# Performance work log

Hardware: AMD Instinct MI355X
Metric: run time of the kernel (lower is better)

Reference implementation:

```python
import jax, jax.numpy as jnp
import numpy as np

B, S, E, H = 1, 2048, 1024, 16
D = E // H          # head_dim = 64
SM_SCALE = 0.5      # module default, not 1/sqrt(D)


def setup_inputs() -> dict:
    key = jax.random.key(0)
    ks = jax.random.split(key, 9)
    std = 0.02
    return {
        "x":  jax.random.normal(ks[0], (B, S, E), dtype=jnp.float32),
        "Wq": jax.random.normal(ks[1], (E, E), dtype=jnp.float32) * std,
        "bq": jnp.zeros((E,), dtype=jnp.float32),
        "Wk": jax.random.normal(ks[2], (E, E), dtype=jnp.float32) * std,
        "bk": jnp.zeros((E,), dtype=jnp.float32),
        "Wv": jax.random.normal(ks[3], (E, E), dtype=jnp.float32) * std,
        "bv": jnp.zeros((E,), dtype=jnp.float32),
        "Wo": jax.random.normal(ks[4], (E, E), dtype=jnp.float32) * std,
        "bo": jnp.zeros((E,), dtype=jnp.float32),
    }


def _split_heads(t):
    # [B,S,E] -> [B,H,S,D]
    b, s, _ = t.shape
    return jnp.transpose(t.reshape(b, s, H, D), (0, 2, 1, 3))


def reference(x, Wq, bq, Wk, bk, Wv, bv, Wo, bo):
    # Projections in fp32, then cast to bf16 (matches module's .astype(bf16))
    q = _split_heads((x @ Wq + bq).astype(jnp.bfloat16))
    k = _split_heads((x @ Wk + bk).astype(jnp.bfloat16))
    v = _split_heads((x @ Wv + bv).astype(jnp.bfloat16))

    # Blockwise loop in the original is mathematically full causal attention
    scores = jnp.einsum("bhqd,bhkd->bhqk", q, k) * SM_SCALE  # [B,H,S,S] bf16
    causal = jnp.tril(jnp.ones((S, S), dtype=bool))
    scores = jnp.where(causal[None, None, :, :], scores, -jnp.inf)
    probs = jax.nn.softmax(scores, axis=-1)
    out = jnp.einsum("bhqk,bhkd->bhqd", probs, v)            # [B,H,S,D]

    out = jnp.transpose(out, (0, 2, 1, 3)).reshape(B, S, E)
    # dropout off (is_training=False / rate=0); final projection in fp32
    return out.astype(jnp.float32) @ Wo + bo
```

## Files before the change

### kernel.cpp

```cpp
#include <hip/hip_runtime.h>
#include <hip/hip_bf16.h>

#define S_LEN 2048
#define E_DIM 1024
#define NH    16
#define HD    64
#define SM_SCALE 0.5f

typedef short bf16x8_t __attribute__((ext_vector_type(8)));
typedef float f32x4_t  __attribute__((ext_vector_type(4)));
typedef __bf16 bf16x4_t __attribute__((ext_vector_type(4)));

static __device__ __forceinline__ unsigned short f2bf_bits(float f) {
    return __builtin_bit_cast(unsigned short, (__bf16)f);
}

#define GLD16(gp, lp) __builtin_amdgcn_global_load_lds(                       \
    (const __attribute__((address_space(1))) void*)(gp),                      \
    (__attribute__((address_space(3))) void*)(lp), 16, 0, 0)

__global__ void k_prep(const float* __restrict__ x,
                       const float* __restrict__ Wq, const float* __restrict__ Wk,
                       const float* __restrict__ Wv, const float* __restrict__ Wo,
                       __bf16* __restrict__ xb, __bf16* __restrict__ wt) {
    const int z = blockIdx.z;
    if (z < 4) {
        __shared__ float tile[32][33];
        const float* W = z == 0 ? Wq : z == 1 ? Wk : z == 2 ? Wv : Wo;
        __bf16* o = wt + (size_t)z * E_DIM * E_DIM;
        const int tx = threadIdx.x, ty = threadIdx.y;
        const int bx = blockIdx.x * 32, by = blockIdx.y * 32;
#pragma unroll
        for (int j = 0; j < 32; j += 8)
            tile[ty + j][tx] = W[(size_t)(by + ty + j) * E_DIM + bx + tx];
        __syncthreads();
#pragma unroll
        for (int j = 0; j < 32; j += 8)
            o[(size_t)(bx + ty + j) * E_DIM + by + tx] = (__bf16)tile[tx][ty + j];
    } else {
        const int bid = (z - 4) * 1024 + blockIdx.y * 32 + blockIdx.x;
        const int tid = threadIdx.y * 32 + threadIdx.x;
        const int i = bid * 256 + tid;
        const float4 v = ((const float4*)x)[i];
        bf16x4_t o4;
        o4.x = (__bf16)v.x; o4.y = (__bf16)v.y; o4.z = (__bf16)v.z; o4.w = (__bf16)v.w;
        ((bf16x4_t*)xb)[i] = o4;
    }
}

__global__ __launch_bounds__(256) void k_gemm_qkv(
    const __bf16* __restrict__ xb, const __bf16* __restrict__ wt,
    const float* __restrict__ bq, const float* __restrict__ bk, const float* __restrict__ bv,
    __bf16* __restrict__ qkv) {
    __shared__ __align__(16) unsigned short As[64 * 32];
    __shared__ __align__(16) unsigned short Bs[128 * 32];

    const int z = blockIdx.z;
    const __bf16* Bt = wt + (size_t)z * E_DIM * E_DIM;
    const float* bias = z == 0 ? bq : z == 1 ? bk : bv;
    __bf16* out = qkv + (size_t)z * NH * S_LEN * HD;

    const int tid = threadIdx.x, w = tid >> 6, l = tid & 63;
    const int lm = l & 15, q4 = l >> 4;
    const int bm = blockIdx.y, bn = blockIdx.x;
    const int wm = w >> 1, wn = w & 1;

    const int sm = (w << 4) + (l >> 2);
    const int skk = (l & 3) << 3;
    const __bf16* Ag = xb + (size_t)(bm * 64 + sm) * E_DIM + skk;
    const __bf16* Bg = Bt + (size_t)(bn * 128 + sm) * E_DIM + skk;
    unsigned short* AsW = As + (w << 9);
    unsigned short* BsW = Bs + (w << 9);

    f32x4_t acc[2][4];
#pragma unroll
    for (int i = 0; i < 2; i++)
#pragma unroll
        for (int j = 0; j < 4; j++) { acc[i][j].x = 0.f; acc[i][j].y = 0.f; acc[i][j].z = 0.f; acc[i][j].w = 0.f; }

    for (int k0 = 0; k0 < E_DIM; k0 += 32) {
        __syncthreads();
        GLD16(Ag + k0, AsW);
        GLD16(Bg + k0, BsW);
        GLD16(Bg + (size_t)64 * E_DIM + k0, BsW + 2048);
        __syncthreads();

        bf16x8_t af[2], bfr[4];
#pragma unroll
        for (int mt = 0; mt < 2; mt++)
            af[mt] = *(const bf16x8_t*)&As[(wm * 32 + mt * 16 + lm) * 32 + q4 * 8];
#pragma unroll
        for (int nt = 0; nt < 4; nt++)
            bfr[nt] = *(const bf16x8_t*)&Bs[(wn * 64 + nt * 16 + lm) * 32 + q4 * 8];
#pragma unroll
        for (int mt = 0; mt < 2; mt++)
#pragma unroll
            for (int nt = 0; nt < 4; nt++)
                acc[mt][nt] = __builtin_amdgcn_mfma_f32_16x16x32_bf16(af[mt], bfr[nt], acc[mt][nt], 0, 0, 0);
    }

#pragma unroll
    for (int nt = 0; nt < 4; nt++) {
        const int n = bn * 128 + wn * 64 + nt * 16 + lm;
        const float bval = bias[n];
        const int h = n >> 6, d = n & 63;
        if (z == 2) {
            __bf16* ob = out + (size_t)h * HD * S_LEN + (size_t)d * S_LEN;
#pragma unroll
            for (int mt = 0; mt < 2; mt++) {
                const int r0 = bm * 64 + wm * 32 + mt * 16 + q4 * 4;
                union { unsigned short s[4]; uint2 u; } pk;
#pragma unroll
                for (int i = 0; i < 4; i++) pk.s[i] = f2bf_bits(acc[mt][nt][i] + bval);
                *(uint2*)(ob + r0) = pk.u;
            }
        } else {
            const float scale = (z == 0) ? SM_SCALE : 1.0f;
            __bf16* ob = out + (size_t)h * S_LEN * HD + d;
#pragma unroll
            for (int mt = 0; mt < 2; mt++) {
                const int r0 = bm * 64 + wm * 32 + mt * 16 + q4 * 4;
#pragma unroll
                for (int i = 0; i < 4; i++)
                    ob[(size_t)(r0 + i) * HD] = (__bf16)((acc[mt][nt][i] + bval) * scale);
            }
        }
    }
}

__global__ __launch_bounds__(256, 2) void k_attn(
    const __bf16* __restrict__ Q, const __bf16* __restrict__ K, const __bf16* __restrict__ Vt,
    __bf16* __restrict__ attn) {
    __shared__ __align__(16) unsigned short KV[4 * 4096];
    __shared__ __align__(16) unsigned short Pl[4][32 * 72];

    const int b = blockIdx.x;
    int qt, h;
    if (b < 256) { qt = 16 + (b >> 4); h = b & 15; }
    else         { qt = 15 - ((b - 256) >> 4); h = (b - 256) & 15; }

    const int tid = threadIdx.x, w = tid >> 6, l = tid & 63;
    const int p = w & 1;
    const int rh = w >> 1;
    const int lm = l & 15, q4 = l >> 4;

    const __bf16* Qb = Q + (size_t)h * S_LEN * HD;
    const __bf16* Kb = K + (size_t)h * S_LEN * HD;
    const __bf16* Vb = Vt + (size_t)h * HD * S_LEN;

    const int qrow0 = qt * 64 + rh * 32;

    bf16x8_t qf[2][2];
#pragma unroll
    for (int rg = 0; rg < 2; rg++)
#pragma unroll
        for (int c = 0; c < 2; c++)
            qf[rg][c] = *(const bf16x8_t*)(Qb + (size_t)(qrow0 + rg * 16 + lm) * HD + c * 32 + q4 * 8);

    float lacc[2][4];
    f32x4_t oacc[2][4];
#pragma unroll
    for (int rg = 0; rg < 2; rg++)
#pragma unroll
        for (int i = 0; i < 4; i++) lacc[rg][i] = 0.f;
#pragma unroll
    for (int rg = 0; rg < 2; rg++)
#pragma unroll
        for (int t = 0; t < 4; t++) { oacc[rg][t].x = 0.f; oacc[rg][t].y = 0.f; oacc[rg][t].z = 0.f; oacc[rg][t].w = 0.f; }

    unsigned short* Pw = Pl[w];
    unsigned short* stg = KV + (w << 12);
    const int swz = (l & 7) ^ (l >> 3);

    const int nsteps = qt / 2 + 1;
    for (int s = 0; s < nsteps; s++) {
        __syncthreads();
        {
            const int tkt = 2 * s + (w & 1);
            if (w < 2) {
                const __bf16* gp = Kb + (size_t)tkt * 64 * HD;
#pragma unroll
                for (int i = 0; i < 8; i++)
                    GLD16(gp + (size_t)(i * 8 + (l >> 3)) * HD + swz * 8,
                          stg + i * 512 + l * 8);
            } else {
                const __bf16* gp = Vb + (size_t)tkt * 64;
#pragma unroll
                for (int i = 0; i < 8; i++)
                    GLD16(gp + (size_t)(i * 8 + (l >> 3)) * S_LEN + swz * 8,
                          stg + i * 512 + l * 8);
            }
        }
        __syncthreads();

        const int kt = 2 * s + p;
        if (kt > qt) continue;
        const unsigned short* Ksp = KV + p * 4096;
        const unsigned short* Vsp = KV + (2 + p) * 4096;

        f32x4_t sc[2][4];
#pragma unroll
        for (int rg = 0; rg < 2; rg++)
#pragma unroll
            for (int t = 0; t < 4; t++) { sc[rg][t].x = 0.f; sc[rg][t].y = 0.f; sc[rg][t].z = 0.f; sc[rg][t].w = 0.f; }
#pragma unroll
        for (int t = 0; t < 4; t++) {
            const int row = t * 16 + lm;
            bf16x8_t kf0 = *(const bf16x8_t*)&Ksp[row * 64 + ((q4 ^ (lm & 7)) << 3)];
            bf16x8_t kf1 = *(const bf16x8_t*)&Ksp[row * 64 + (((4 + q4) ^ (lm & 7)) << 3)];
            sc[0][t] = __builtin_amdgcn_mfma_f32_16x16x32_bf16(qf[0][0], kf0, sc[0][t], 0, 0, 0);
            sc[0][t] = __builtin_amdgcn_mfma_f32_16x16x32_bf16(qf[0][1], kf1, sc[0][t], 0, 0, 0);
            sc[1][t] = __builtin_amdgcn_mfma_f32_16x16x32_bf16(qf[1][0], kf0, sc[1][t], 0, 0, 0);
            sc[1][t] = __builtin_amdgcn_mfma_f32_16x16x32_bf16(qf[1][1], kf1, sc[1][t], 0, 0, 0);
        }
        if (kt == qt) {
#pragma unroll
            for (int rg = 0; rg < 2; rg++)
#pragma unroll
                for (int t = 0; t < 4; t++) {
                    const int kcol = kt * 64 + t * 16 + lm;
#pragma unroll
                    for (int i = 0; i < 4; i++) {
                        const int qrow = qrow0 + rg * 16 + q4 * 4 + i;
                        sc[rg][t][i] = (kcol > qrow) ? 0.f : __expf(sc[rg][t][i]);
                    }
                }
        } else {
#pragma unroll
            for (int rg = 0; rg < 2; rg++)
#pragma unroll
                for (int t = 0; t < 4; t++)
#pragma unroll
                    for (int i = 0; i < 4; i++) sc[rg][t][i] = __expf(sc[rg][t][i]);
        }
#pragma unroll
        for (int rg = 0; rg < 2; rg++)
#pragma unroll
            for (int i = 0; i < 4; i++)
                lacc[rg][i] += (sc[rg][0][i] + sc[rg][1][i]) + (sc[rg][2][i] + sc[rg][3][i]);
#pragma unroll
        for (int rg = 0; rg < 2; rg++)
#pragma unroll
            for (int t = 0; t < 4; t++)
#pragma unroll
                for (int i = 0; i < 4; i++)
                    Pw[(rg * 16 + q4 * 4 + i) * 72 + t * 16 + lm] = f2bf_bits(sc[rg][t][i]);
#pragma unroll
        for (int c = 0; c < 2; c++) {
            bf16x8_t pf0 = *(const bf16x8_t*)&Pw[lm * 72 + c * 32 + q4 * 8];
            bf16x8_t pf1 = *(const bf16x8_t*)&Pw[(16 + lm) * 72 + c * 32 + q4 * 8];
#pragma unroll
            for (int t = 0; t < 4; t++) {
                bf16x8_t vf = *(const bf16x8_t*)&Vsp[(t * 16 + lm) * 64 + ((((c << 2) + q4) ^ (lm & 7)) << 3)];
                oacc[0][t] = __builtin_amdgcn_mfma_f32_16x16x32_bf16(pf0, vf, oacc[0][t], 0, 0, 0);
                oacc[1][t] = __builtin_amdgcn_mfma_f32_16x16x32_bf16(pf1, vf, oacc[1][t], 0, 0, 0);
            }
        }
    }

    __syncthreads();
    float* Ex = (float*)KV;
    float* Ll = (float*)Pl;
    if (p == 1) {
#pragma unroll
        for (int rg = 0; rg < 2; rg++)
#pragma unroll
            for (int t = 0; t < 4; t++)
#pragma unroll
                for (int i = 0; i < 4; i++) {
                    const int idx = rg * 16 + t * 4 + i;
                    Ex[(rh * 64 + l) * 32 + ((idx + l) & 31)] = oacc[rg][t][i];
                }
#pragma unroll
        for (int rg = 0; rg < 2; rg++)
#pragma unroll
            for (int i = 0; i < 4; i++)
                Ll[(rh * 64 + l) * 8 + rg * 4 + i] = lacc[rg][i];
    }
    __syncthreads();
    if (p == 0) {
#pragma unroll
        for (int rg = 0; rg < 2; rg++)
#pragma unroll
            for (int t = 0; t < 4; t++)
#pragma unroll
                for (int i = 0; i < 4; i++) {
                    const int idx = rg * 16 + t * 4 + i;
                    oacc[rg][t][i] += Ex[(rh * 64 + l) * 32 + ((idx + l) & 31)];
                }
#pragma unroll
        for (int rg = 0; rg < 2; rg++)
#pragma unroll
            for (int i = 0; i < 4; i++)
                lacc[rg][i] += Ll[(rh * 64 + l) * 8 + rg * 4 + i];
#pragma unroll
        for (int off = 1; off <= 8; off <<= 1)
#pragma unroll
            for (int rg = 0; rg < 2; rg++)
#pragma unroll
                for (int i = 0; i < 4; i++)
                    lacc[rg][i] += __shfl_xor(lacc[rg][i], off, 64);
#pragma unroll
        for (int rg = 0; rg < 2; rg++)
#pragma unroll
            for (int i = 0; i < 4; i++) {
                const float rl = 1.f / lacc[rg][i];
                const int row = qrow0 + rg * 16 + q4 * 4 + i;
#pragma unroll
                for (int t = 0; t < 4; t++)
                    attn[(size_t)row * E_DIM + h * HD + t * 16 + lm] = (__bf16)(oacc[rg][t][i] * rl);
            }
    }
}

__global__ __launch_bounds__(256) void k_gemm_out(
    const __bf16* __restrict__ A, const __bf16* __restrict__ Bt,
    const float* __restrict__ bias, float* __restrict__ out) {
    __shared__ __align__(16) unsigned short As[64 * 32];
    __shared__ __align__(16) unsigned short Bs[128 * 32];

    const int tid = threadIdx.x, w = tid >> 6, l = tid & 63;
    const int lm = l & 15, q4 = l >> 4;
    const int bm = blockIdx.y, bn = blockIdx.x;
    const int wm = w >> 1, wn = w & 1;

    const int sm = (w << 4) + (l >> 2);
    const int skk = (l & 3) << 3;
    const __bf16* Ag = A + (size_t)(bm * 64 + sm) * E_DIM + skk;
    const __bf16* Bg = Bt + (size_t)(bn * 128 + sm) * E_DIM + skk;
    unsigned short* AsW = As + (w << 9);
    unsigned short* BsW = Bs + (w << 9);

    f32x4_t acc[2][4];
#pragma unroll
    for (int i = 0; i < 2; i++)
#pragma unroll
        for (int j = 0; j < 4; j++) { acc[i][j].x = 0.f; acc[i][j].y = 0.f; acc[i][j].z = 0.f; acc[i][j].w = 0.f; }

    for (int k0 = 0; k0 < E_DIM; k0 += 32) {
        __syncthreads();
        GLD16(Ag + k0, AsW);
        GLD16(Bg + k0, BsW);
        GLD16(Bg + (size_t)64 * E_DIM + k0, BsW + 2048);
        __syncthreads();

        bf16x8_t af[2], bfr[4];
#pragma unroll
        for (int mt = 0; mt < 2; mt++)
            af[mt] = *(const bf16x8_t*)&As[(wm * 32 + mt * 16 + lm) * 32 + q4 * 8];
#pragma unroll
        for (int nt = 0; nt < 4; nt++)
            bfr[nt] = *(const bf16x8_t*)&Bs[(wn * 64 + nt * 16 + lm) * 32 + q4 * 8];
#pragma unroll
        for (int mt = 0; mt < 2; mt++)
#pragma unroll
            for (int nt = 0; nt < 4; nt++)
                acc[mt][nt] = __builtin_amdgcn_mfma_f32_16x16x32_bf16(af[mt], bfr[nt], acc[mt][nt], 0, 0, 0);
    }

#pragma unroll
    for (int nt = 0; nt < 4; nt++) {
        const int n = bn * 128 + wn * 64 + nt * 16 + lm;
        const float bval = bias[n];
#pragma unroll
        for (int mt = 0; mt < 2; mt++) {
            const int r0 = bm * 64 + wm * 32 + mt * 16 + q4 * 4;
#pragma unroll
            for (int i = 0; i < 4; i++)
                out[(size_t)(r0 + i) * E_DIM + n] = acc[mt][nt][i] + bval;
        }
    }
}

extern "C" void kernel_launch(void* const* d_in, const int* in_sizes, int n_in,
                              void* d_out, int out_size, void* d_ws, size_t ws_size,
                              hipStream_t stream) {
    const float* x  = (const float*)d_in[0];
    const float* Wq = (const float*)d_in[1];
    const float* bq = (const float*)d_in[2];
    const float* Wk = (const float*)d_in[3];
    const float* bk = (const float*)d_in[4];
    const float* Wv = (const float*)d_in[5];
    const float* bv = (const float*)d_in[6];
    const float* Wo = (const float*)d_in[7];
    const float* bo = (const float*)d_in[8];
    float* out = (float*)d_out;

    char* ws = (char*)d_ws;
    __bf16* xb   = (__bf16*)(ws);
    __bf16* wt   = (__bf16*)(ws + ((size_t)4  << 20));
    __bf16* qkv  = (__bf16*)(ws + ((size_t)12 << 20));
    __bf16* attn = (__bf16*)(ws + ((size_t)24 << 20));

    k_prep<<<dim3(32, 32, 6), dim3(32, 8), 0, stream>>>(x, Wq, Wk, Wv, Wo, xb, wt);
    k_gemm_qkv<<<dim3(E_DIM / 128, S_LEN / 64, 3), 256, 0, stream>>>(xb, wt, bq, bk, bv, qkv);
    k_attn<<<dim3(512), 256, 0, stream>>>(
        qkv, qkv + (size_t)NH * S_LEN * HD, qkv + (size_t)2 * NH * S_LEN * HD, attn);
    k_gemm_out<<<dim3(E_DIM / 128, S_LEN / 64), 256, 0, stream>>>(
        attn, wt + (size_t)3 * E_DIM * E_DIM, bo, out);
}
```

Baseline: 154.5 us.

## Write Q/K/V in MFMA fragment order and load attention operands directly from global

The projection kernel now stores Q, K and V in a tiled layout that matches the MFMA fragment order, so each lane's 8-element operand is one contiguous 16-byte chunk. The attention kernel drops the LDS staging of K/V tiles and the two block-wide barriers per step, loading K and V fragments straight from global memory (L2-resident) per wave. LDS use falls, and launch bounds go from 2 to 4 blocks per CU to raise occupancy. The trade-off is that global-load latency is exposed inside the inner loop, and the two wave pairs each re-read the same K/V tiles instead of sharing them through LDS.

Result: slower. 195.0 us (+26.2%).

```diff
diff --git a/kernel.cpp b/kernel.cpp
--- a/kernel.cpp
+++ b/kernel.cpp
@@ -105,34 +105,40 @@
         const float bval = bias[n];
         const int h = n >> 6, d = n & 63;
         if (z == 2) {
-            __bf16* ob = out + (size_t)h * HD * S_LEN + (size_t)d * S_LEN;
+            const int t4 = d >> 4, flm = d & 15;
 #pragma unroll
             for (int mt = 0; mt < 2; mt++) {
-                const int r0 = bm * 64 + wm * 32 + mt * 16 + q4 * 4;
+                const int q4p = (mt * 2 + (q4 >> 1)) & 3;
+                const int j0 = (q4 & 1) * 4;
+                __bf16* ob = out + ((((size_t)h * 32 + bm) * 4 + t4) * 2 + wm) * 512
+                                 + (q4p * 16 + flm) * 8 + j0;
                 union { unsigned short s[4]; uint2 u; } pk;
 #pragma unroll
                 for (int i = 0; i < 4; i++) pk.s[i] = f2bf_bits(acc[mt][nt][i] + bval);
-                *(uint2*)(ob + r0) = pk.u;
+                *(uint2*)ob = pk.u;
             }
         } else {
             const float scale = (z == 0) ? SM_SCALE : 1.0f;
-            __bf16* ob = out + (size_t)h * S_LEN * HD + d;
+            const int c = d >> 5, q4p = (d >> 3) & 3, j = d & 7;
 #pragma unroll
             for (int mt = 0; mt < 2; mt++) {
-                const int r0 = bm * 64 + wm * 32 + mt * 16 + q4 * 4;
+                const int s0 = bm * 64 + wm * 32 + mt * 16;
+                const int kt6 = s0 >> 6, t4 = (s0 >> 4) & 3;
+                __bf16* ob = out + ((((size_t)h * 32 + kt6) * 4 + t4) * 2 + c) * 512
+                                 + (q4p * 16 + q4 * 4) * 8 + j;
 #pragma unroll
                 for (int i = 0; i < 4; i++)
-                    ob[(size_t)(r0 + i) * HD] = (__bf16)((acc[mt][nt][i] + bval) * scale);
+                    ob[i * 8] = (__bf16)((acc[mt][nt][i] + bval) * scale);
             }
         }
     }
 }
 
-__global__ __launch_bounds__(256, 2) void k_attn(
-    const __bf16* __restrict__ Q, const __bf16* __restrict__ K, const __bf16* __restrict__ Vt,
+__global__ __launch_bounds__(256, 4) void k_attn(
+    const __bf16* __restrict__ Qf, const __bf16* __restrict__ Kf, const __bf16* __restrict__ Vf,
     __bf16* __restrict__ attn) {
-    __shared__ __align__(16) unsigned short KV[4 * 4096];
     __shared__ __align__(16) unsigned short Pl[4][32 * 72];
+    __shared__ float Ll[2][64][8];
 
     const int b = blockIdx.x;
     int qt, h;
@@ -144,9 +150,9 @@
     const int rh = w >> 1;
     const int lm = l & 15, q4 = l >> 4;
 
-    const __bf16* Qb = Q + (size_t)h * S_LEN * HD;
-    const __bf16* Kb = K + (size_t)h * S_LEN * HD;
-    const __bf16* Vb = Vt + (size_t)h * HD * S_LEN;
+    const __bf16* Qb = Qf + ((size_t)h * 32 + qt) * 4096;
+    const __bf16* Kb = Kf + (size_t)h * 32 * 4096;
+    const __bf16* Vb = Vf + (size_t)h * 32 * 4096;
 
     const int qrow0 = qt * 64 + rh * 32;
 
@@ -155,7 +161,7 @@
     for (int rg = 0; rg < 2; rg++)
 #pragma unroll
         for (int c = 0; c < 2; c++)
-            qf[rg][c] = *(const bf16x8_t*)(Qb + (size_t)(qrow0 + rg * 16 + lm) * HD + c * 32 + q4 * 8);
+            qf[rg][c] = *(const bf16x8_t*)(Qb + (((rh * 2 + rg) * 2 + c) << 9) + l * 8);
 
     float lacc[2][4];
     f32x4_t oacc[2][4];
@@ -169,89 +175,49 @@
         for (int t = 0; t < 4; t++) { oacc[rg][t].x = 0.f; oacc[rg][t].y = 0.f; oacc[rg][t].z = 0.f; oacc[rg][t].w = 0.f; }
 
     unsigned short* Pw = Pl[w];
-    unsigned short* stg = KV + (w << 12);
-    const int swz = (l & 7) ^ (l >> 3);
-
-    const int nsteps = qt / 2 + 1;
-    for (int s = 0; s < nsteps; s++) {
-        __syncthreads();
-        {
-            const int tkt = 2 * s + (w & 1);
-            if (w < 2) {
-                const __bf16* gp = Kb + (size_t)tkt * 64 * HD;
-#pragma unroll
-                for (int i = 0; i < 8; i++)
-                    GLD16(gp + (size_t)(i * 8 + (l >> 3)) * HD + swz * 8,
-                          stg + i * 512 + l * 8);
+
+    for (int kt = p; kt <= qt; kt += 2) {
+        const __bf16* Kt = Kb + (size_t)kt * 4096;
+        const __bf16* Vt = Vb + (size_t)kt * 4096;
+        const bool diag = (kt == qt);
+#pragma unroll
+        for (int t = 0; t < 4; t++) {
+            bf16x8_t kf0 = *(const bf16x8_t*)(Kt + ((t * 2 + 0) << 9) + l * 8);
+            bf16x8_t kf1 = *(const bf16x8_t*)(Kt + ((t * 2 + 1) << 9) + l * 8);
+            f32x4_t s0, s1;
+            s0.x = 0.f; s0.y = 0.f; s0.z = 0.f; s0.w = 0.f;
+            s1 = s0;
+            s0 = __builtin_amdgcn_mfma_f32_16x16x32_bf16(qf[0][0], kf0, s0, 0, 0, 0);
+            s0 = __builtin_amdgcn_mfma_f32_16x16x32_bf16(qf[0][1], kf1, s0, 0, 0, 0);
+            s1 = __builtin_amdgcn_mfma_f32_16x16x32_bf16(qf[1][0], kf0, s1, 0, 0, 0);
+            s1 = __builtin_amdgcn_mfma_f32_16x16x32_bf16(qf[1][1], kf1, s1, 0, 0, 0);
+            if (diag) {
+                const int kcol = kt * 64 + t * 16 + lm;
+#pragma unroll
+                for (int i = 0; i < 4; i++) {
+                    const int qr = qrow0 + q4 * 4 + i;
+                    s0[i] = (kcol > qr) ? 0.f : __expf(s0[i]);
+                    s1[i] = (kcol > qr + 16) ? 0.f : __expf(s1[i]);
+                }
             } else {
-                const __bf16* gp = Vb + (size_t)tkt * 64;
-#pragma unroll
-                for (int i = 0; i < 8; i++)
-                    GLD16(gp + (size_t)(i * 8 + (l >> 3)) * S_LEN + swz * 8,
-                          stg + i * 512 + l * 8);
+#pragma unroll
+                for (int i = 0; i < 4; i++) { s0[i] = __expf(s0[i]); s1[i] = __expf(s1[i]); }
+            }
+#pragma unroll
+            for (int i = 0; i < 4; i++) {
+                lacc[0][i] += s0[i];
+                lacc[1][i] += s1[i];
+                Pw[(q4 * 4 + i) * 72 + t * 16 + lm] = f2bf_bits(s0[i]);
+                Pw[(16 + q4 * 4 + i) * 72 + t * 16 + lm] = f2bf_bits(s1[i]);
             }
         }
-        __syncthreads();
-
-        const int kt = 2 * s + p;
-        if (kt > qt) continue;
-        const unsigned short* Ksp = KV + p * 4096;
-        const unsigned short* Vsp = KV + (2 + p) * 4096;
-
-        f32x4_t sc[2][4];
-#pragma unroll
-        for (int rg = 0; rg < 2; rg++)
-#pragma unroll
-            for (int t = 0; t < 4; t++) { sc[rg][t].x = 0.f; sc[rg][t].y = 0.f; sc[rg][t].z = 0.f; sc[rg][t].w = 0.f; }
-#pragma unroll
-        for (int t = 0; t < 4; t++) {
-            const int row = t * 16 + lm;
-            bf16x8_t kf0 = *(const bf16x8_t*)&Ksp[row * 64 + ((q4 ^ (lm & 7)) << 3)];
-            bf16x8_t kf1 = *(const bf16x8_t*)&Ksp[row * 64 + (((4 + q4) ^ (lm & 7)) << 3)];
-            sc[0][t] = __builtin_amdgcn_mfma_f32_16x16x32_bf16(qf[0][0], kf0, sc[0][t], 0, 0, 0);
-            sc[0][t] = __builtin_amdgcn_mfma_f32_16x16x32_bf16(qf[0][1], kf1, sc[0][t], 0, 0, 0);
-            sc[1][t] = __builtin_amdgcn_mfma_f32_16x16x32_bf16(qf[1][0], kf0, sc[1][t], 0, 0, 0);
-            sc[1][t] = __builtin_amdgcn_mfma_f32_16x16x32_bf16(qf[1][1], kf1, sc[1][t], 0, 0, 0);
-        }
-        if (kt == qt) {
-#pragma unroll
-            for (int rg = 0; rg < 2; rg++)
-#pragma unroll
-                for (int t = 0; t < 4; t++) {
-                    const int kcol = kt * 64 + t * 16 + lm;
-#pragma unroll
-                    for (int i = 0; i < 4; i++) {
-                        const int qrow = qrow0 + rg * 16 + q4 * 4 + i;
-                        sc[rg][t][i] = (kcol > qrow) ? 0.f : __expf(sc[rg][t][i]);
-                    }
-                }
-        } else {
-#pragma unroll
-            for (int rg = 0; rg < 2; rg++)
-#pragma unroll
-                for (int t = 0; t < 4; t++)
-#pragma unroll
-                    for (int i = 0; i < 4; i++) sc[rg][t][i] = __expf(sc[rg][t][i]);
-        }
-#pragma unroll
-        for (int rg = 0; rg < 2; rg++)
-#pragma unroll
-            for (int i = 0; i < 4; i++)
-                lacc[rg][i] += (sc[rg][0][i] + sc[rg][1][i]) + (sc[rg][2][i] + sc[rg][3][i]);
-#pragma unroll
-        for (int rg = 0; rg < 2; rg++)
-#pragma unroll
-            for (int t = 0; t < 4; t++)
-#pragma unroll
-                for (int i = 0; i < 4; i++)
-                    Pw[(rg * 16 + q4 * 4 + i) * 72 + t * 16 + lm] = f2bf_bits(sc[rg][t][i]);
 #pragma unroll
         for (int c = 0; c < 2; c++) {
             bf16x8_t pf0 = *(const bf16x8_t*)&Pw[lm * 72 + c * 32 + q4 * 8];
             bf16x8_t pf1 = *(const bf16x8_t*)&Pw[(16 + lm) * 72 + c * 32 + q4 * 8];
 #pragma unroll
             for (int t = 0; t < 4; t++) {
-                bf16x8_t vf = *(const bf16x8_t*)&Vsp[(t * 16 + lm) * 64 + ((((c << 2) + q4) ^ (lm & 7)) << 3)];
+                bf16x8_t vf = *(const bf16x8_t*)(Vt + ((t * 2 + c) << 9) + l * 8);
                 oacc[0][t] = __builtin_amdgcn_mfma_f32_16x16x32_bf16(pf0, vf, oacc[0][t], 0, 0, 0);
                 oacc[1][t] = __builtin_amdgcn_mfma_f32_16x16x32_bf16(pf1, vf, oacc[1][t], 0, 0, 0);
             }
@@ -259,8 +225,7 @@
     }
 
     __syncthreads();
-    float* Ex = (float*)KV;
-    float* Ll = (float*)Pl;
+    float* Ex = (float*)Pl;
     if (p == 1) {
 #pragma unroll
         for (int rg = 0; rg < 2; rg++)
@@ -275,7 +240,7 @@
         for (int rg = 0; rg < 2; rg++)
 #pragma unroll
             for (int i = 0; i < 4; i++)
-                Ll[(rh * 64 + l) * 8 + rg * 4 + i] = lacc[rg][i];
+                Ll[rh][l][rg * 4 + i] = lacc[rg][i];
     }
     __syncthreads();
     if (p == 0) {
@@ -292,7 +257,7 @@
         for (int rg = 0; rg < 2; rg++)
 #pragma unroll
             for (int i = 0; i < 4; i++)
-                lacc[rg][i] += Ll[(rh * 64 + l) * 8 + rg * 4 + i];
+                lacc[rg][i] += Ll[rh][l][rg * 4 + i];
 #pragma unroll
         for (int off = 1; off <= 8; off <<= 1)
 #pragma unroll
```
